# Performance work log

Measured on AMD Instinct MI355X. Metric: run time of the kernel, lower is better.

Reference implementation:

```python
import jax, jax.numpy as jnp
import numpy as np

N = 50000
E = 800000
G = 2500  # number of graphs


def setup_inputs() -> dict:
    key = jax.random.key(0)
    ks = jax.random.split(key, 10)
    x = jax.random.normal(ks[0], (N, 128), dtype=jnp.float32)
    edge_index = jax.random.randint(ks[1], (2, E), 0, N, dtype=jnp.int64)
    batch = jnp.sort(jax.random.randint(ks[2], (N,), 0, G, dtype=jnp.int64))
    def lin(k, fan_in, shape):
        return jax.random.normal(k, shape, dtype=jnp.float32) / np.sqrt(fan_in)
    return {
        'x': x, 'edge_index': edge_index, 'batch': batch,
        'W1': lin(ks[3], 128, (128, 64)), 'b1': jnp.zeros((64,), jnp.float32),
        'W2': lin(ks[4], 64, (64, 64)),  'b2': jnp.zeros((64,), jnp.float32),
        'W3': lin(ks[5], 64, (64, 64)),  'b3': jnp.zeros((64,), jnp.float32),
        'Wp1': lin(ks[6], 64, (64, 64)), 'bp1': jnp.zeros((64,), jnp.float32),
        'Wp2': lin(ks[7], 64, (64, 32)), 'bp2': jnp.zeros((32,), jnp.float32),
    }


def _gcn_norm(edge_index, n_nodes):
    # PyG GCNConv default: add self-loops, symmetric normalization
    loops = jnp.arange(n_nodes, dtype=edge_index.dtype)
    src = jnp.concatenate([edge_index[0], loops])
    dst = jnp.concatenate([edge_index[1], loops])
    deg = jax.ops.segment_sum(jnp.ones_like(dst, dtype=jnp.float32), dst,
                              num_segments=n_nodes)
    dis = jnp.where(deg > 0, jax.lax.rsqrt(deg), 0.0)
    norm = dis[src] * dis[dst]  # [E + N]
    return src, dst, norm


def _gcn_conv(x, W, b, src, dst, norm, n_nodes):
    h = x @ W                                   # transform first (small dim)
    m = h[src] * norm[:, None]                  # gather + scale
    out = jax.ops.segment_sum(m, dst, num_segments=n_nodes)  # scatter-add
    return out + b


def reference(x, edge_index, batch, W1, b1, W2, b2, W3, b3, Wp1, bp1, Wp2, bp2):
    n_nodes = x.shape[0]
    src, dst, norm = _gcn_norm(edge_index, n_nodes)
    x1 = jax.nn.relu(_gcn_conv(x, W1, b1, src, dst, norm, n_nodes))
    x2 = jax.nn.relu(_gcn_conv(x1, W2, b2, src, dst, norm, n_nodes))
    x3 = jax.nn.relu(_gcn_conv(x2, W3, b3, src, dst, norm, n_nodes))
    h = x1 + x2 + x3
    # global_mean_pool
    sums = jax.ops.segment_sum(h, batch, num_segments=G)
    counts = jax.ops.segment_sum(jnp.ones((n_nodes,), jnp.float32), batch,
                                 num_segments=G)
    pooled = sums / jnp.maximum(counts, 1.0)[:, None]
    z = jax.nn.relu(pooled @ Wp1 + bp1) @ Wp2 + bp2
    return z
```

## Files before the change

### kernel.cpp

```cpp
#include <hip/hip_runtime.h>
#include <math.h>


typedef short short8 __attribute__((ext_vector_type(8)));
typedef float f32x4 __attribute__((ext_vector_type(4)));

__device__ inline float bf2f(unsigned short h) {
    return __uint_as_float((unsigned)h << 16);
}
__device__ inline unsigned short f2bf(float f) {
    unsigned u = __float_as_uint(f);
    return (unsigned short)((u + (0x7FFFu + ((u >> 16) & 1u))) >> 16);
}
__device__ inline void bh8f(short8 u, float4& a, float4& b) {
    a.x = bf2f((unsigned short)u[0]); a.y = bf2f((unsigned short)u[1]);
    a.z = bf2f((unsigned short)u[2]); a.w = bf2f((unsigned short)u[3]);
    b.x = bf2f((unsigned short)u[4]); b.y = bf2f((unsigned short)u[5]);
    b.z = bf2f((unsigned short)u[6]); b.w = bf2f((unsigned short)u[7]);
}
__device__ inline float4 f4add(float4 a, float4 acc) {
    acc.x += a.x; acc.y += a.y; acc.z += a.z; acc.w += a.w;
    return acc;
}

template <int K>
__global__ __launch_bounds__(256) void k_hist_gemm(const int* __restrict__ dst,
                                                   int* __restrict__ hist, int E, int chunk,
                                                   const float* __restrict__ X,
                                                   const float* __restrict__ W,
                                                   unsigned short* __restrict__ H, int n) {
    __shared__ int hh[256];
    __shared__ short wt[64 * K];
    int t = threadIdx.x;
    if (blockIdx.x < 256) {
        hh[t] = 0;
        __syncthreads();
        int e0 = blockIdx.x * chunk;
        int e1 = min(e0 + chunk, E);
        for (int e = e0 + t; e < e1; e += 256) atomicAdd(&hh[dst[e] >> 8], 1);
        __syncthreads();
        hist[blockIdx.x * 256 + t] = hh[t];
        return;
    }
    for (int idx = t; idx < 64 * K; idx += 256) {
        int k = idx >> 6, ch = idx & 63;
        wt[ch * K + k] = (short)f2bf(W[idx]);
    }
    __syncthreads();
    int wave = t >> 6, lane = t & 63;
    int q = lane >> 4, l = lane & 15;
    int tile = (blockIdx.x - 256) * 4 + wave;
    if (tile * 16 >= n) return;
    int node = tile * 16 + l;
    short8 afr[4][K / 32];
#pragma unroll
    for (int mb = 0; mb < 4; mb++)
#pragma unroll
        for (int s = 0; s < K / 32; s++)
            afr[mb][s] = *(const short8*)(wt + (mb * 16 + l) * K + s * 32 + q * 8);
    f32x4 acc[4] = {};
    const float* xr = X + (size_t)node * K + q * 8;
#pragma unroll
    for (int s = 0; s < K / 32; s++) {
        float4 xa = *(const float4*)(xr + s * 32);
        float4 xb = *(const float4*)(xr + s * 32 + 4);
        short8 bfr;
        bfr[0] = (short)f2bf(xa.x); bfr[1] = (short)f2bf(xa.y);
        bfr[2] = (short)f2bf(xa.z); bfr[3] = (short)f2bf(xa.w);
        bfr[4] = (short)f2bf(xb.x); bfr[5] = (short)f2bf(xb.y);
        bfr[6] = (short)f2bf(xb.z); bfr[7] = (short)f2bf(xb.w);
#pragma unroll
        for (int mb = 0; mb < 4; mb++)
            acc[mb] = __builtin_amdgcn_mfma_f32_16x16x32_bf16(afr[mb][s], bfr, acc[mb], 0, 0, 0);
    }
#pragma unroll
    for (int mb = 0; mb < 4; mb++) {
        ushort4 u;
        u.x = f2bf(acc[mb][0]); u.y = f2bf(acc[mb][1]);
        u.z = f2bf(acc[mb][2]); u.w = f2bf(acc[mb][3]);
        ((ushort4*)H)[(size_t)node * 16 + mb * 4 + q] = u;
    }
}

__global__ void kA_colscan(const int* __restrict__ hist, int* __restrict__ cursorA,
                           int* __restrict__ tot, float* __restrict__ pooled, int PG) {
    __shared__ int s[256];
    int t = threadIdx.x;
    int k = blockIdx.x;
    int v = hist[t * 256 + k];
    s[t] = v;
    __syncthreads();
    for (int st = 1; st < 256; st <<= 1) {
        int u = s[t];
        if (t >= st) u += s[t - st];
        __syncthreads();
        s[t] = u;
        __syncthreads();
    }
    cursorA[t * 256 + k] = s[t] - v;
    if (t == 255) tot[k] = s[255];
    for (int i = k * 256 + t; i < PG; i += 65536) pooled[i] = 0.f;
}

__global__ void kA_scatter(const int* __restrict__ src, const int* __restrict__ dst,
                           const int* __restrict__ cursorA, const int* __restrict__ tot,
                           unsigned* __restrict__ ebuf, int E, int chunk) {
    __shared__ int s[256];
    __shared__ int cur[256];
    int t = threadIdx.x;
    s[t] = tot[t];
    __syncthreads();
    for (int st = 1; st < 256; st <<= 1) {
        int u = s[t];
        if (t >= st) u += s[t - st];
        __syncthreads();
        s[t] = u;
        __syncthreads();
    }
    int bstart = (t == 0) ? 0 : s[t - 1];
    cur[t] = cursorA[blockIdx.x * 256 + t] + bstart;
    __syncthreads();
    int e0 = blockIdx.x * chunk;
    int e1 = min(e0 + chunk, E);
    for (int e = e0 + t; e < e1; e += 256) {
        int d = dst[e];
        int p = atomicAdd(&cur[d >> 8], 1);
        ebuf[p] = ((unsigned)(d & 255) << 24) | (unsigned)src[e];
    }
}

__global__ void kB(const unsigned* __restrict__ ebuf, const int* __restrict__ tot,
                   float* __restrict__ dis, int* __restrict__ offsP,
                   unsigned* __restrict__ col, unsigned short* __restrict__ Hb,
                   unsigned short* __restrict__ Hb2, int N, int ZR) {
    __shared__ int s[256];
    __shared__ int h[256];
    __shared__ int cur[256];
    __shared__ float sdis[256];
    int t = threadIdx.x;
    int k = blockIdx.x;
    s[t] = tot[t];
    __syncthreads();
    for (int st = 1; st < 256; st <<= 1) {
        int u = s[t];
        if (t >= st) u += s[t - st];
        __syncthreads();
        s[t] = u;
        __syncthreads();
    }
    int lo = (k == 0) ? 0 : s[k - 1];
    int hi = s[k];
    int padbase = ((lo + 3) & ~3) + 768 * k;
    h[t] = 0;
    __syncthreads();
    for (int p = lo + t; p < hi; p += 256) atomicAdd(&h[ebuf[p] >> 24], 1);
    __syncthreads();
    int c = h[t];
    int cp = (c + 3) & ~3;
    int node = k * 256 + t;
    float dn = rsqrtf((float)(c + 1));
    sdis[t] = dn;
    if (node < N) dis[node] = dn;
    s[t] = cp;
    __syncthreads();
    for (int st = 1; st < 256; st <<= 1) {
        int u = s[t];
        if (t >= st) u += s[t - st];
        __syncthreads();
        s[t] = u;
        __syncthreads();
    }
    int start = padbase + s[t] - cp;
    if (node < N) offsP[node] = (start << 9) | cp;
    cur[t] = start;
    __syncthreads();
    for (int p = lo + t; p < hi; p += 256) {
        unsigned e = ebuf[p];
        int q = atomicAdd(&cur[e >> 24], 1);
        col[q] = e & 0x00FFFFFFu;
    }
    __syncthreads();
    if (node < N) {
        int end = start + cp;
        for (int q = cur[t]; q < end; q++) col[q] = (unsigned)ZR;
    }
    for (int idx = t; idx < 2048; idx += 256) {
        int nl = idx >> 3, cs = idx & 7;
        int nd = k * 256 + nl;
        if (nd >= N) continue;
        float d2 = sdis[nl];
        short8 v = ((const short8*)Hb)[(size_t)nd * 8 + cs];
        float4 a, b;
        bh8f(v, a, b);
        short8 o;
        o[0] = (short)f2bf(a.x * d2); o[1] = (short)f2bf(a.y * d2);
        o[2] = (short)f2bf(a.z * d2); o[3] = (short)f2bf(a.w * d2);
        o[4] = (short)f2bf(b.x * d2); o[5] = (short)f2bf(b.y * d2);
        o[6] = (short)f2bf(b.z * d2); o[7] = (short)f2bf(b.w * d2);
        ((short8*)Hb)[(size_t)nd * 8 + cs] = o;
    }
    if (k == 0) {
        if (t < 32) ((unsigned*)Hb)[(size_t)ZR * 32 + t] = 0u;
        else if (t < 64) ((unsigned*)Hb2)[(size_t)ZR * 32 + (t - 32)] = 0u;
    }
}

__global__ __launch_bounds__(256) void k_aggemm(const unsigned short* __restrict__ H,
                                                const unsigned* __restrict__ col,
                                                const int* __restrict__ offsP,
                                                const float* __restrict__ dis,
                                                const float* __restrict__ bias,
                                                const float* __restrict__ W,
                                                unsigned short* __restrict__ Xout,
                                                unsigned short* __restrict__ Hout, int n) {
    __shared__ short wt[64 * 64];
    __shared__ short vbuf[32 * 72];
    int t = threadIdx.x;
    for (int idx = t; idx < 64 * 64; idx += 256) {
        int k = idx >> 6, ch = idx & 63;
        wt[ch * 64 + k] = (short)f2bf(W[idx]);
    }
    const short8* Hs = (const short8*)H;
    int base = blockIdx.x * 32;
    int cs = t & 7;
    int nl = t >> 3;
    int node = base + nl;
    const float4* bias4 = (const float4*)bias;
    float4 bb0 = bias4[cs * 2];
    float4 bb1 = bias4[cs * 2 + 1];
    if (node < n) {
        float dn = dis[node];
        float4 acc0, acc1;
        bh8f(Hs[(size_t)node * 8 + cs], acc0, acc1);
        int po = offsP[node];
        int p = po >> 9, hiP = p + (po & 511);
        for (; p + 8 <= hiP; p += 8) {
            uint4 ea = *(const uint4*)(col + p);
            uint4 eb = *(const uint4*)(col + p + 4);
            short8 g0 = Hs[(size_t)ea.x * 8 + cs];
            short8 g1 = Hs[(size_t)ea.y * 8 + cs];
            short8 g2 = Hs[(size_t)ea.z * 8 + cs];
            short8 g3 = Hs[(size_t)ea.w * 8 + cs];
            short8 g4 = Hs[(size_t)eb.x * 8 + cs];
            short8 g5 = Hs[(size_t)eb.y * 8 + cs];
            short8 g6 = Hs[(size_t)eb.z * 8 + cs];
            short8 g7 = Hs[(size_t)eb.w * 8 + cs];
            float4 a, b;
            bh8f(g0, a, b); acc0 = f4add(a, acc0); acc1 = f4add(b, acc1);
            bh8f(g1, a, b); acc0 = f4add(a, acc0); acc1 = f4add(b, acc1);
            bh8f(g2, a, b); acc0 = f4add(a, acc0); acc1 = f4add(b, acc1);
            bh8f(g3, a, b); acc0 = f4add(a, acc0); acc1 = f4add(b, acc1);
            bh8f(g4, a, b); acc0 = f4add(a, acc0); acc1 = f4add(b, acc1);
            bh8f(g5, a, b); acc0 = f4add(a, acc0); acc1 = f4add(b, acc1);
            bh8f(g6, a, b); acc0 = f4add(a, acc0); acc1 = f4add(b, acc1);
            bh8f(g7, a, b); acc0 = f4add(a, acc0); acc1 = f4add(b, acc1);
        }
        if (p < hiP) {
            uint4 e4 = *(const uint4*)(col + p);
            short8 g0 = Hs[(size_t)e4.x * 8 + cs];
            short8 g1 = Hs[(size_t)e4.y * 8 + cs];
            short8 g2 = Hs[(size_t)e4.z * 8 + cs];
            short8 g3 = Hs[(size_t)e4.w * 8 + cs];
            float4 a, b;
            bh8f(g0, a, b); acc0 = f4add(a, acc0); acc1 = f4add(b, acc1);
            bh8f(g1, a, b); acc0 = f4add(a, acc0); acc1 = f4add(b, acc1);
            bh8f(g2, a, b); acc0 = f4add(a, acc0); acc1 = f4add(b, acc1);
            bh8f(g3, a, b); acc0 = f4add(a, acc0); acc1 = f4add(b, acc1);
        }
        float4 v0, v1;
        v0.x = fmaxf(acc0.x * dn + bb0.x, 0.f);
        v0.y = fmaxf(acc0.y * dn + bb0.y, 0.f);
        v0.z = fmaxf(acc0.z * dn + bb0.z, 0.f);
        v0.w = fmaxf(acc0.w * dn + bb0.w, 0.f);
        v1.x = fmaxf(acc1.x * dn + bb1.x, 0.f);
        v1.y = fmaxf(acc1.y * dn + bb1.y, 0.f);
        v1.z = fmaxf(acc1.z * dn + bb1.z, 0.f);
        v1.w = fmaxf(acc1.w * dn + bb1.w, 0.f);
        short8 o;
        o[0] = (short)f2bf(v0.x); o[1] = (short)f2bf(v0.y);
        o[2] = (short)f2bf(v0.z); o[3] = (short)f2bf(v0.w);
        o[4] = (short)f2bf(v1.x); o[5] = (short)f2bf(v1.y);
        o[6] = (short)f2bf(v1.z); o[7] = (short)f2bf(v1.w);
        ((short8*)Xout)[(size_t)node * 8 + cs] = o;
        *(short8*)(vbuf + nl * 72 + cs * 8) = o;
    }
    __syncthreads();
    int wave = t >> 6, lane = t & 63;
    if (wave >= 2) return;
    int q = lane >> 4, l = lane & 15;
    if (base + wave * 16 >= n) return;
    int mnode = base + wave * 16 + l;
    float dn2 = dis[mnode];
    short8 afr[4][2];
#pragma unroll
    for (int mb = 0; mb < 4; mb++)
#pragma unroll
        for (int s = 0; s < 2; s++)
            afr[mb][s] = *(const short8*)(wt + (mb * 16 + l) * 64 + s * 32 + q * 8);
    f32x4 acc[4] = {};
#pragma unroll
    for (int s = 0; s < 2; s++) {
        short8 bfr = *(const short8*)(vbuf + (wave * 16 + l) * 72 + s * 32 + q * 8);
#pragma unroll
        for (int mb = 0; mb < 4; mb++)
            acc[mb] = __builtin_amdgcn_mfma_f32_16x16x32_bf16(afr[mb][s], bfr, acc[mb], 0, 0, 0);
    }
#pragma unroll
    for (int mb = 0; mb < 4; mb++) {
        ushort4 u;
        u.x = f2bf(acc[mb][0] * dn2); u.y = f2bf(acc[mb][1] * dn2);
        u.z = f2bf(acc[mb][2] * dn2); u.w = f2bf(acc[mb][3] * dn2);
        ((ushort4*)Hout)[(size_t)mnode * 16 + mb * 4 + q] = u;
    }
}

__global__ __launch_bounds__(256) void k_agg3pool(const unsigned short* __restrict__ H,
                                                  const unsigned* __restrict__ col,
                                                  const int* __restrict__ offsP,
                                                  const float* __restrict__ dis,
                                                  const float* __restrict__ bias,
                                                  const unsigned short* __restrict__ add1,
                                                  const unsigned short* __restrict__ add2,
                                                  const int* __restrict__ batch,
                                                  float* __restrict__ pooled, int n) {
    __shared__ float sm[32][65];
    __shared__ int sg[32];
    int t = threadIdx.x;
    int base = blockIdx.x * 32;
    int nl = t >> 3, lane = t & 7;
    int node = base + nl;
    if (t < 32) sg[t] = (base + t < n) ? batch[base + t] : -1;
    if (node < n) {
        const short8* Hs = (const short8*)H;
        float dn = dis[node];
        float4 acc0, acc1;
        bh8f(Hs[(size_t)node * 8 + lane], acc0, acc1);
        int po = offsP[node];
        int p = po >> 9, hiP = p + (po & 511);
        for (; p + 8 <= hiP; p += 8) {
            uint4 ea = *(const uint4*)(col + p);
            uint4 eb = *(const uint4*)(col + p + 4);
            short8 g0 = Hs[(size_t)ea.x * 8 + lane];
            short8 g1 = Hs[(size_t)ea.y * 8 + lane];
            short8 g2 = Hs[(size_t)ea.z * 8 + lane];
            short8 g3 = Hs[(size_t)ea.w * 8 + lane];
            short8 g4 = Hs[(size_t)eb.x * 8 + lane];
            short8 g5 = Hs[(size_t)eb.y * 8 + lane];
            short8 g6 = Hs[(size_t)eb.z * 8 + lane];
            short8 g7 = Hs[(size_t)eb.w * 8 + lane];
            float4 a, b;
            bh8f(g0, a, b); acc0 = f4add(a, acc0); acc1 = f4add(b, acc1);
            bh8f(g1, a, b); acc0 = f4add(a, acc0); acc1 = f4add(b, acc1);
            bh8f(g2, a, b); acc0 = f4add(a, acc0); acc1 = f4add(b, acc1);
            bh8f(g3, a, b); acc0 = f4add(a, acc0); acc1 = f4add(b, acc1);
            bh8f(g4, a, b); acc0 = f4add(a, acc0); acc1 = f4add(b, acc1);
            bh8f(g5, a, b); acc0 = f4add(a, acc0); acc1 = f4add(b, acc1);
            bh8f(g6, a, b); acc0 = f4add(a, acc0); acc1 = f4add(b, acc1);
            bh8f(g7, a, b); acc0 = f4add(a, acc0); acc1 = f4add(b, acc1);
        }
        if (p < hiP) {
            uint4 e4 = *(const uint4*)(col + p);
            short8 g0 = Hs[(size_t)e4.x * 8 + lane];
            short8 g1 = Hs[(size_t)e4.y * 8 + lane];
            short8 g2 = Hs[(size_t)e4.z * 8 + lane];
            short8 g3 = Hs[(size_t)e4.w * 8 + lane];
            float4 a, b;
            bh8f(g0, a, b); acc0 = f4add(a, acc0); acc1 = f4add(b, acc1);
            bh8f(g1, a, b); acc0 = f4add(a, acc0); acc1 = f4add(b, acc1);
            bh8f(g2, a, b); acc0 = f4add(a, acc0); acc1 = f4add(b, acc1);
            bh8f(g3, a, b); acc0 = f4add(a, acc0); acc1 = f4add(b, acc1);
        }
        const float4* bias4 = (const float4*)bias;
        float4 bb0 = bias4[lane * 2];
        float4 bb1 = bias4[lane * 2 + 1];
        float4 v0, v1;
        v0.x = fmaxf(acc0.x * dn + bb0.x, 0.f);
        v0.y = fmaxf(acc0.y * dn + bb0.y, 0.f);
        v0.z = fmaxf(acc0.z * dn + bb0.z, 0.f);
        v0.w = fmaxf(acc0.w * dn + bb0.w, 0.f);
        v1.x = fmaxf(acc1.x * dn + bb1.x, 0.f);
        v1.y = fmaxf(acc1.y * dn + bb1.y, 0.f);
        v1.z = fmaxf(acc1.z * dn + bb1.z, 0.f);
        v1.w = fmaxf(acc1.w * dn + bb1.w, 0.f);
        size_t slot = (size_t)node * 8 + lane;
        float4 a10, a11, a20, a21;
        bh8f(((const short8*)add1)[slot], a10, a11);
        bh8f(((const short8*)add2)[slot], a20, a21);
        v0.x += a10.x + a20.x; v0.y += a10.y + a20.y;
        v0.z += a10.z + a20.z; v0.w += a10.w + a20.w;
        v1.x += a11.x + a21.x; v1.y += a11.y + a21.y;
        v1.z += a11.z + a21.z; v1.w += a11.w + a21.w;
        float* r = &sm[nl][lane * 8];
        r[0] = v0.x; r[1] = v0.y; r[2] = v0.z; r[3] = v0.w;
        r[4] = v1.x; r[5] = v1.y; r[6] = v1.z; r[7] = v1.w;
    }
    __syncthreads();
    if (t < 64) {
        float acc = 0.f;
        int cg = -1;
        for (int i = 0; i < 32; i++) {
            int g = sg[i];
            if (g != cg) {
                if (cg >= 0) atomicAdd(&pooled[(size_t)cg * 64 + t], acc);
                cg = g;
                acc = 0.f;
            }
            if (g >= 0) acc += sm[i][t];
        }
        if (cg >= 0) atomicAdd(&pooled[(size_t)cg * 64 + t], acc);
    }
}

__global__ void k_head(const float* __restrict__ pooled, const int* __restrict__ batch,
                       const float* __restrict__ Wp1, const float* __restrict__ bp1,
                       const float* __restrict__ Wp2, const float* __restrict__ bp2,
                       float* __restrict__ out, int n, int G) {
    int g = blockIdx.x;
    int j = threadIdx.x;
    int a = 0, b = n;
    while (a < b) { int m = (a + b) >> 1; if (batch[m] < g) a = m + 1; else b = m; }
    int beg = a;
    b = n;
    while (a < b) { int m = (a + b) >> 1; if (batch[m] < g + 1) a = m + 1; else b = m; }
    int end = a;
    float cnt = (float)(end - beg);
    float p = pooled[(size_t)g * 64 + j] / fmaxf(cnt, 1.f);
    __shared__ float ps[64];
    __shared__ float ts[64];
    ps[j] = p;
    __syncthreads();
    float t1 = bp1[j];
#pragma unroll 8
    for (int k = 0; k < 64; k++) t1 += ps[k] * Wp1[k * 64 + j];
    t1 = fmaxf(t1, 0.f);
    ts[j] = t1;
    __syncthreads();
    if (j < 32) {
        float o = bp2[j];
#pragma unroll 8
        for (int k = 0; k < 64; k++) o += ts[k] * Wp2[k * 32 + j];
        out[(size_t)g * 32 + j] = o;
    }
}

extern "C" void kernel_launch(void* const* d_in, const int* in_sizes, int n_in,
                              void* d_out, int out_size, void* d_ws, size_t ws_size,
                              hipStream_t stream) {
    const float* x   = (const float*)d_in[0];
    const int*   ei  = (const int*)d_in[1];
    const int*   bat = (const int*)d_in[2];
    const float* W1  = (const float*)d_in[3];
    const float* b1  = (const float*)d_in[4];
    const float* W2  = (const float*)d_in[5];
    const float* b2  = (const float*)d_in[6];
    const float* W3  = (const float*)d_in[7];
    const float* b3  = (const float*)d_in[8];
    const float* Wp1 = (const float*)d_in[9];
    const float* bp1 = (const float*)d_in[10];
    const float* Wp2 = (const float*)d_in[11];
    const float* bp2 = (const float*)d_in[12];

    int N = in_sizes[0] / 128;
    int E = in_sizes[1] / 2;
    int G = out_size / 32;
    const int* src = ei;
    const int* dst = ei + E;

    char* w = (char*)d_ws;
    auto alloc = [&](size_t bytes) -> void* {
        void* p = (void*)w;
        w += (bytes + 255) & ~(size_t)255;
        return p;
    };
    int NB = (N + 255) / 256;
    int ZR = N;
    int*            offsP   = (int*)alloc((size_t)N * 4);
    unsigned*       col     = (unsigned*)alloc(((size_t)E + 3 * (size_t)N + 2048) * 4);
    float*          dis     = (float*)alloc((size_t)N * 4);
    int*            hist    = (int*)alloc((size_t)256 * 256 * 4);
    int*            cursorA = (int*)alloc((size_t)256 * 256 * 4);
    int*            tot     = (int*)alloc((size_t)256 * 4);
    unsigned*       ebuf    = (unsigned*)alloc((size_t)E * 4);
    unsigned short* Hb      = (unsigned short*)alloc(((size_t)N + 16) * 64 * 2);
    unsigned short* Hb2     = (unsigned short*)alloc(((size_t)N + 16) * 64 * 2);
    unsigned short* X1      = (unsigned short*)alloc((size_t)N * 64 * 2);
    unsigned short* X2      = (unsigned short*)alloc((size_t)N * 64 * 2);
    float*          pooled  = (float*)alloc((size_t)G * 64 * 4);

    int chunk = (E + 255) / 256;
    int ggemm = ((N >> 4) + 3) / 4;
    int gfuse = (N + 31) / 32;
    int gagg  = (N + 31) / 32;

    k_hist_gemm<128><<<256 + ggemm, 256, 0, stream>>>(dst, hist, E, chunk, x, W1, Hb, N);
    kA_colscan<<<256, 256, 0, stream>>>(hist, cursorA, tot, pooled, G * 64);
    kA_scatter<<<256, 256, 0, stream>>>(src, dst, cursorA, tot, ebuf, E, chunk);
    kB<<<NB, 256, 0, stream>>>(ebuf, tot, dis, offsP, col, Hb, Hb2, N, ZR);

    k_aggemm<<<gfuse, 256, 0, stream>>>(Hb, col, offsP, dis, b1, W2, X1, Hb2, N);
    k_aggemm<<<gfuse, 256, 0, stream>>>(Hb2, col, offsP, dis, b2, W3, X2, Hb, N);
    k_agg3pool<<<gagg, 256, 0, stream>>>(Hb, col, offsP, dis, b3, X1, X2, bat, pooled, N);

    k_head<<<G, 64, 0, stream>>>(pooled, bat, Wp1, bp1, Wp2, bp2, (float*)d_out, N, G);
}
```

Measured before the change: 209.8 us.

## Pool each layer's activations inside aggregation kernels instead of storing X1/X2

```diff
diff --git a/kernel.cpp b/kernel.cpp
--- a/kernel.cpp
+++ b/kernel.cpp
@@ -211,10 +211,13 @@
                                                 const float* __restrict__ dis,
                                                 const float* __restrict__ bias,
                                                 const float* __restrict__ W,
-                                                unsigned short* __restrict__ Xout,
+                                                const int* __restrict__ batch,
+                                                float* __restrict__ pooled,
                                                 unsigned short* __restrict__ Hout, int n) {
     __shared__ short wt[64 * 64];
     __shared__ short vbuf[32 * 72];
+    __shared__ float sm[32][65];
+    __shared__ int sg[32];
     int t = threadIdx.x;
     for (int idx = t; idx < 64 * 64; idx += 256) {
         int k = idx >> 6, ch = idx & 63;
@@ -225,6 +228,7 @@
     int cs = t & 7;
     int nl = t >> 3;
     int node = base + nl;
+    if (t < 32) sg[t] = (base + t < n) ? batch[base + t] : -1;
     const float4* bias4 = (const float4*)bias;
     float4 bb0 = bias4[cs * 2];
     float4 bb1 = bias4[cs * 2 + 1];
@@ -281,11 +285,29 @@
         o[2] = (short)f2bf(v0.z); o[3] = (short)f2bf(v0.w);
         o[4] = (short)f2bf(v1.x); o[5] = (short)f2bf(v1.y);
         o[6] = (short)f2bf(v1.z); o[7] = (short)f2bf(v1.w);
-        ((short8*)Xout)[(size_t)node * 8 + cs] = o;
         *(short8*)(vbuf + nl * 72 + cs * 8) = o;
+        float* r = &sm[nl][cs * 8];
+        r[0] = v0.x; r[1] = v0.y; r[2] = v0.z; r[3] = v0.w;
+        r[4] = v1.x; r[5] = v1.y; r[6] = v1.z; r[7] = v1.w;
     }
     __syncthreads();
     int wave = t >> 6, lane = t & 63;
+    if (wave == 3) {
+        int c = t - 192;
+        float acc = 0.f;
+        int cg = -1;
+        for (int i = 0; i < 32; i++) {
+            int g = sg[i];
+            if (g != cg) {
+                if (cg >= 0) atomicAdd(&pooled[(size_t)cg * 64 + c], acc);
+                cg = g;
+                acc = 0.f;
+            }
+            if (g >= 0) acc += sm[i][c];
+        }
+        if (cg >= 0) atomicAdd(&pooled[(size_t)cg * 64 + c], acc);
+        return;
+    }
     if (wave >= 2) return;
     int q = lane >> 4, l = lane & 15;
     if (base + wave * 16 >= n) return;
@@ -319,8 +341,6 @@
                                                   const int* __restrict__ offsP,
                                                   const float* __restrict__ dis,
                                                   const float* __restrict__ bias,
-                                                  const unsigned short* __restrict__ add1,
-                                                  const unsigned short* __restrict__ add2,
                                                   const int* __restrict__ batch,
                                                   float* __restrict__ pooled, int n) {
     __shared__ float sm[32][65];
@@ -373,26 +393,15 @@
         const float4* bias4 = (const float4*)bias;
         float4 bb0 = bias4[lane * 2];
         float4 bb1 = bias4[lane * 2 + 1];
-        float4 v0, v1;
-        v0.x = fmaxf(acc0.x * dn + bb0.x, 0.f);
-        v0.y = fmaxf(acc0.y * dn + bb0.y, 0.f);
-        v0.z = fmaxf(acc0.z * dn + bb0.z, 0.f);
-        v0.w = fmaxf(acc0.w * dn + bb0.w, 0.f);
-        v1.x = fmaxf(acc1.x * dn + bb1.x, 0.f);
-        v1.y = fmaxf(acc1.y * dn + bb1.y, 0.f);
-        v1.z = fmaxf(acc1.z * dn + bb1.z, 0.f);
-        v1.w = fmaxf(acc1.w * dn + bb1.w, 0.f);
-        size_t slot = (size_t)node * 8 + lane;
-        float4 a10, a11, a20, a21;
-        bh8f(((const short8*)add1)[slot], a10, a11);
-        bh8f(((const short8*)add2)[slot], a20, a21);
-        v0.x += a10.x + a20.x; v0.y += a10.y + a20.y;
-        v0.z += a10.z + a20.z; v0.w += a10.w + a20.w;
-        v1.x += a11.x + a21.x; v1.y += a11.y + a21.y;
-        v1.z += a11.z + a21.z; v1.w += a11.w + a21.w;
         float* r = &sm[nl][lane * 8];
-        r[0] = v0.x; r[1] = v0.y; r[2] = v0.z; r[3] = v0.w;
-        r[4] = v1.x; r[5] = v1.y; r[6] = v1.z; r[7] = v1.w;
+        r[0] = fmaxf(acc0.x * dn + bb0.x, 0.f);
+        r[1] = fmaxf(acc0.y * dn + bb0.y, 0.f);
+        r[2] = fmaxf(acc0.z * dn + bb0.z, 0.f);
+        r[3] = fmaxf(acc0.w * dn + bb0.w, 0.f);
+        r[4] = fmaxf(acc1.x * dn + bb1.x, 0.f);
+        r[5] = fmaxf(acc1.y * dn + bb1.y, 0.f);
+        r[6] = fmaxf(acc1.z * dn + bb1.z, 0.f);
+        r[7] = fmaxf(acc1.w * dn + bb1.w, 0.f);
     }
     __syncthreads();
     if (t < 64) {
@@ -483,8 +492,6 @@
     unsigned*       ebuf    = (unsigned*)alloc((size_t)E * 4);
     unsigned short* Hb      = (unsigned short*)alloc(((size_t)N + 16) * 64 * 2);
     unsigned short* Hb2     = (unsigned short*)alloc(((size_t)N + 16) * 64 * 2);
-    unsigned short* X1      = (unsigned short*)alloc((size_t)N * 64 * 2);
-    unsigned short* X2      = (unsigned short*)alloc((size_t)N * 64 * 2);
     float*          pooled  = (float*)alloc((size_t)G * 64 * 4);
 
     int chunk = (E + 255) / 256;
@@ -497,9 +504,9 @@
     kA_scatter<<<256, 256, 0, stream>>>(src, dst, cursorA, tot, ebuf, E, chunk);
     kB<<<NB, 256, 0, stream>>>(ebuf, tot, dis, offsP, col, Hb, Hb2, N, ZR);
 
-    k_aggemm<<<gfuse, 256, 0, stream>>>(Hb, col, offsP, dis, b1, W2, X1, Hb2, N);
-    k_aggemm<<<gfuse, 256, 0, stream>>>(Hb2, col, offsP, dis, b2, W3, X2, Hb, N);
-    k_agg3pool<<<gagg, 256, 0, stream>>>(Hb, col, offsP, dis, b3, X1, X2, bat, pooled, N);
+    k_aggemm<<<gfuse, 256, 0, stream>>>(Hb, col, offsP, dis, b1, W2, bat, pooled, Hb2, N);
+    k_aggemm<<<gfuse, 256, 0, stream>>>(Hb2, col, offsP, dis, b2, W3, bat, pooled, Hb, N);
+    k_agg3pool<<<gagg, 256, 0, stream>>>(Hb, col, offsP, dis, b3, bat, pooled, N);
 
     k_head<<<G, 64, 0, stream>>>(pooled, bat, Wp1, bp1, Wp2, bp2, (float*)d_out, N, G);
 }
```

Result: no change. 213.7 us (+1.9%).
